# Kernel optimization log

Measured on AMD Instinct MI355X. Metric: run time of the kernel, lower is better.

## Reference

```python
import jax, jax.numpy as jnp
import numpy as np

N_NODES = 100000
N_EDGES = 1600000
D_IN = 64
D_OUT = 64


def setup_inputs() -> dict:
    key = jax.random.key(0)
    k1, k2, k3, k4 = jax.random.split(key, 4)
    x = jax.random.normal(k1, (N_NODES, D_IN), dtype=jnp.float32)
    W = jax.random.normal(k2, (D_OUT, D_IN), dtype=jnp.float32) * 0.1
    b = jax.random.normal(k3, (D_OUT,), dtype=jnp.float32) * 0.1
    edge_index = jax.random.randint(k4, (2, N_EDGES), 0, N_NODES, dtype=jnp.int64 if jax.config.jax_enable_x64 else jnp.int32)
    return {"x": x, "W": W, "b": b, "edge_index": edge_index}


def reference(x, W, b, edge_index):
    N = x.shape[0]
    # add self loops
    loop = jnp.arange(N, dtype=edge_index.dtype)
    src = jnp.concatenate([edge_index[0], loop])  # row: source nodes
    dst = jnp.concatenate([edge_index[1], loop])  # col: target nodes
    E = src.shape[0]

    # linear transform
    h = x @ W.T + b  # [N, D_OUT]

    # degree over source (row) indices, as in the original message()
    ones = jnp.ones((E,), dtype=h.dtype)
    deg = jax.ops.segment_sum(ones, src, num_segments=N)  # [N]
    deg_inv_sqrt = jnp.where(deg > 0, jax.lax.rsqrt(jnp.maximum(deg, 1.0)), 0.0)
    norm = deg_inv_sqrt[src] * deg_inv_sqrt[dst]  # [E]

    # gather-scale messages, then scatter-mean into targets
    msg = norm[:, None] * h[src]  # [E, D_OUT]
    agg_sum = jax.ops.segment_sum(msg, dst, num_segments=N)  # [N, D_OUT]
    cnt = jax.ops.segment_sum(ones, dst, num_segments=N)  # [N]
    out = agg_sum / jnp.maximum(cnt, 1.0)[:, None]
    return out
```

## Files before the change

### kernel.cpp

```cpp
#include <hip/hip_runtime.h>
#include <hip/hip_fp16.h>

#define N_D 64
#define PB_D 6
#define PSZ_D 64
#define CAP_D 1536
#define PB_S 7
#define PSZ_S 128
#define CAP_S 3072

__global__ __launch_bounds__(1024) void scatter_kernel(const int* __restrict__ src,
                                                       const int* __restrict__ dst,
                                                       int* __restrict__ cursorD,
                                                       int* __restrict__ cursorS,
                                                       unsigned* __restrict__ epart,
                                                       unsigned char* __restrict__ spart,
                                                       int E, int PD, int PS) {
    extern __shared__ int sh[];
    int* hD = sh;
    int* hS = sh + PD;
    int* bD = sh + PD + PS;
    int* bS = sh + 2 * PD + PS;
    int t = threadIdx.x;
    for (int i = t; i < PD + PS; i += 1024) sh[i] = 0;
    __syncthreads();
    const int4* src4 = (const int4*)src;
    const int4* dst4 = (const int4*)dst;
    int E4 = E >> 2;
    int per = (E4 + gridDim.x - 1) / gridDim.x;
    int beg = blockIdx.x * per, end = min(E4, beg + per);
    bool tailblk = (blockIdx.x == 0);
    for (int e = beg + t; e < end; e += 1024) {
        int4 d = dst4[e];
        int4 s = src4[e];
        atomicAdd(&hD[d.x >> PB_D], 1);
        atomicAdd(&hD[d.y >> PB_D], 1);
        atomicAdd(&hD[d.z >> PB_D], 1);
        atomicAdd(&hD[d.w >> PB_D], 1);
        atomicAdd(&hS[s.x >> PB_S], 1);
        atomicAdd(&hS[s.y >> PB_S], 1);
        atomicAdd(&hS[s.z >> PB_S], 1);
        atomicAdd(&hS[s.w >> PB_S], 1);
    }
    if (tailblk) {
        for (int e = (E4 << 2) + t; e < E; e += 1024) {
            atomicAdd(&hD[dst[e] >> PB_D], 1);
            atomicAdd(&hS[src[e] >> PB_S], 1);
        }
    }
    __syncthreads();
    for (int p = t; p < PD; p += 1024) {
        int hd = hD[p];
        if (hd) {
            int r = atomicAdd(&cursorD[p], hd);
            if (r > CAP_D - hd) r = max(CAP_D - hd, 0);
            bD[p] = r;
        }
        hD[p] = 0;
    }
    for (int p = t; p < PS; p += 1024) {
        int hs_ = hS[p];
        if (hs_) {
            int r = atomicAdd(&cursorS[p], hs_);
            if (r > CAP_S - hs_) r = max(CAP_S - hs_, 0);
            bS[p] = r;
        }
        hS[p] = 0;
    }
    __syncthreads();
    for (int e = beg + t; e < end; e += 1024) {
        int4 dv = dst4[e];
        int4 sv = src4[e];
        int ds_[4] = {dv.x, dv.y, dv.z, dv.w};
        int ss_[4] = {sv.x, sv.y, sv.z, sv.w};
#pragma unroll
        for (int k = 0; k < 4; k++) {
            int d = ds_[k], s0 = ss_[k];
            int pd = d >> PB_D, ps = s0 >> PB_S;
            int od = atomicAdd(&hD[pd], 1);
            epart[(size_t)pd * CAP_D + bD[pd] + od] =
                ((unsigned)s0 << PB_D) | (unsigned)(d & (PSZ_D - 1));
            int os = atomicAdd(&hS[ps], 1);
            spart[(size_t)ps * CAP_S + bS[ps] + os] = (unsigned char)(s0 & (PSZ_S - 1));
        }
    }
    if (tailblk) {
        for (int e = (E4 << 2) + t; e < E; e += 1024) {
            int d = dst[e], s0 = src[e];
            int pd = d >> PB_D, ps = s0 >> PB_S;
            int od = atomicAdd(&hD[pd], 1);
            epart[(size_t)pd * CAP_D + bD[pd] + od] =
                ((unsigned)s0 << PB_D) | (unsigned)(d & (PSZ_D - 1));
            int os = atomicAdd(&hS[ps], 1);
            spart[(size_t)ps * CAP_S + bS[ps] + os] = (unsigned char)(s0 & (PSZ_S - 1));
        }
    }
}

#define LROWS 128
__global__ __launch_bounds__(256) void linear_kernel(const float* __restrict__ x,
                                                     const float* __restrict__ W,
                                                     const float* __restrict__ b,
                                                     const unsigned char* __restrict__ spart,
                                                     const int* __restrict__ cursorS,
                                                     float* __restrict__ dis,
                                                     __half* __restrict__ hs, int N) {
    __shared__ float xs[LROWS][N_D + 1];
    __shared__ float Wt[N_D][N_D + 4];
    __shared__ float bs[N_D];
    __shared__ int ohist[PSZ_S];
    __shared__ float disS[PSZ_S];

    int tid = threadIdx.x;
    int p = blockIdx.x;
    if (tid < PSZ_S) ohist[tid] = 0;
    for (int i = tid; i < N_D * N_D; i += 256) {
        int o = i >> 6, k = i & 63;
        Wt[k][o] = W[i];
    }
    if (tid < N_D) bs[tid] = b[tid];
    __syncthreads();

    {
        size_t sbase = (size_t)p * CAP_S;
        int len = min(cursorS[p], CAP_S);
        const unsigned* sp4 = (const unsigned*)(spart + sbase);
        int n4 = len >> 2;
        for (int i = tid; i < n4; i += 256) {
            unsigned v = sp4[i];
            atomicAdd(&ohist[v & 127], 1);
            atomicAdd(&ohist[(v >> 8) & 127], 1);
            atomicAdd(&ohist[(v >> 16) & 127], 1);
            atomicAdd(&ohist[(v >> 24) & 127], 1);
        }
        for (int i = (n4 << 2) + tid; i < len; i += 256)
            atomicAdd(&ohist[spart[sbase + i]], 1);
    }

    int row0 = p * LROWS;
    const float4* x4 = (const float4*)(x + (size_t)row0 * N_D);
    const int n4x = LROWS * N_D / 4;
    if (row0 + LROWS <= N) {
        for (int i = tid; i < n4x; i += 256) {
            float4 v = x4[i];
            int r = i >> 4, kq = (i & 15) << 2;
            xs[r][kq] = v.x; xs[r][kq + 1] = v.y; xs[r][kq + 2] = v.z; xs[r][kq + 3] = v.w;
        }
    } else {
        for (int i = tid; i < n4x; i += 256) {
            int r = i >> 4, kq = (i & 15) << 2;
            float4 v = make_float4(0.f, 0.f, 0.f, 0.f);
            if (row0 + r < N) v = x4[i];
            xs[r][kq] = v.x; xs[r][kq + 1] = v.y; xs[r][kq + 2] = v.z; xs[r][kq + 3] = v.w;
        }
    }
    __syncthreads();

    if (tid < PSZ_S) {
        float dv = rsqrtf((float)(ohist[tid] + 1));
        disS[tid] = dv;
        int node = row0 + tid;
        if (node < N) dis[node] = dv;
    }
    __syncthreads();

    int tc = tid >> 5;
    int tr = tid & 31;
    float acc[4][8];
#pragma unroll
    for (int j = 0; j < 4; j++)
#pragma unroll
        for (int i = 0; i < 8; i++) acc[j][i] = 0.f;

#pragma unroll 4
    for (int k = 0; k < N_D; k++) {
        float4 w0 = *(const float4*)&Wt[k][tc * 8];
        float4 w1 = *(const float4*)&Wt[k][tc * 8 + 4];
        float wv[8] = {w0.x, w0.y, w0.z, w0.w, w1.x, w1.y, w1.z, w1.w};
        float xv[4];
#pragma unroll
        for (int j = 0; j < 4; j++) xv[j] = xs[tr + 32 * j][k];
#pragma unroll
        for (int j = 0; j < 4; j++)
#pragma unroll
            for (int i = 0; i < 8; i++) acc[j][i] += xv[j] * wv[i];
    }

#pragma unroll
    for (int j = 0; j < 4; j++) {
        int row = row0 + tr + 32 * j;
        if (row < N) {
            float dr = disS[tr + 32 * j];
            union { __half h[8]; int4 v; } u;
#pragma unroll
            for (int i = 0; i < 8; i++)
                u.h[i] = __float2half_rn((acc[j][i] + bs[tc * 8 + i]) * dr);
            *(int4*)(hs + (size_t)row * N_D + tc * 8) = u.v;
        }
    }
}

__device__ __forceinline__ float hload(const char* hbase, int off, int lane2) {
    return __half2float(*(const __half*)(hbase + (size_t)(unsigned)off + lane2));
}

__global__ __launch_bounds__(256) void gather_part_kernel(const unsigned* __restrict__ epart,
                                                          const int* __restrict__ cursorD,
                                                          const __half* __restrict__ hs,
                                                          const float* __restrict__ dis,
                                                          float* __restrict__ out, int N) {
    __shared__ unsigned raw[CAP_D];
    __shared__ int sorted[CAP_D];
    __shared__ int hist[PSZ_D];
    __shared__ int rs[PSZ_D];
    __shared__ int cur[PSZ_D];
    int p = blockIdx.x, t = threadIdx.x;
    if (t < PSZ_D) hist[t] = 0;
    __syncthreads();
    size_t base = (size_t)p * CAP_D;
    int num = min(cursorD[p], CAP_D);
    {
        const uint4* ep4 = (const uint4*)(epart + base);
        int n4 = num >> 2;
        for (int i4 = t; i4 < n4; i4 += 256) {
            uint4 v = ep4[i4];
            ((uint4*)raw)[i4] = v;
            atomicAdd(&hist[v.x & (PSZ_D - 1)], 1);
            atomicAdd(&hist[v.y & (PSZ_D - 1)], 1);
            atomicAdd(&hist[v.z & (PSZ_D - 1)], 1);
            atomicAdd(&hist[v.w & (PSZ_D - 1)], 1);
        }
        for (int i = (n4 << 2) + t; i < num; i += 256) {
            unsigned e = epart[base + i];
            raw[i] = e;
            atomicAdd(&hist[e & (PSZ_D - 1)], 1);
        }
    }
    __syncthreads();
    int v = 0;
    if (t < PSZ_D) { v = hist[t]; rs[t] = v; }
    __syncthreads();
    for (int off = 1; off < PSZ_D; off <<= 1) {
        int x = 0;
        if (t < PSZ_D && t >= off) x = rs[t - off];
        __syncthreads();
        if (t < PSZ_D) rs[t] += x;
        __syncthreads();
    }
    if (t < PSZ_D) { int ex = rs[t] - v; rs[t] = ex; cur[t] = ex; }
    __syncthreads();
    for (int i = t; i < num; i += 256) {
        unsigned e = raw[i];
        int pos = atomicAdd(&cur[e & (PSZ_D - 1)], 1);
        sorted[pos] = (int)((e & ~(unsigned)(PSZ_D - 1)) << 1);
    }
    __syncthreads();
    int w = t >> 6, lane = t & 63, lane2 = lane << 1;
    const char* hbase = (const char*)hs;
    for (int r = w * 16; r < w * 16 + 16; r++) {
        int node = (p << PB_D) + r;
        if (node >= N) break;
        int jb = rs[r];
        int cnt = hist[r];
        float acc = hload(hbase, node << 7, lane2);
        int j = 0;
        for (; j + 8 <= cnt; j += 8) {
            int o0 = sorted[jb + j + 0], o1 = sorted[jb + j + 1];
            int o2 = sorted[jb + j + 2], o3 = sorted[jb + j + 3];
            int o4 = sorted[jb + j + 4], o5 = sorted[jb + j + 5];
            int o6 = sorted[jb + j + 6], o7 = sorted[jb + j + 7];
            float v0 = hload(hbase, o0, lane2);
            float v1 = hload(hbase, o1, lane2);
            float v2 = hload(hbase, o2, lane2);
            float v3 = hload(hbase, o3, lane2);
            float v4 = hload(hbase, o4, lane2);
            float v5 = hload(hbase, o5, lane2);
            float v6 = hload(hbase, o6, lane2);
            float v7 = hload(hbase, o7, lane2);
            acc += v0; acc += v1; acc += v2; acc += v3;
            acc += v4; acc += v5; acc += v6; acc += v7;
        }
        for (; j < cnt; j++) acc += hload(hbase, sorted[jb + j], lane2);
        out[((size_t)node << 6) + lane] = dis[node] * acc / (float)(cnt + 1);
    }
}

extern "C" void kernel_launch(void* const* d_in, const int* in_sizes, int n_in,
                              void* d_out, int out_size, void* d_ws, size_t ws_size,
                              hipStream_t stream) {
    const float* x = (const float*)d_in[0];
    const float* W = (const float*)d_in[1];
    const float* b = (const float*)d_in[2];
    const int* edge_index = (const int*)d_in[3];

    const int N = in_sizes[0] / N_D;
    const int E = in_sizes[3] / 2;
    const int* src = edge_index;
    const int* dst = edge_index + E;
    float* out = (float*)d_out;

    const int PD = (N + PSZ_D - 1) / PSZ_D;
    const int PS = (N + PSZ_S - 1) / PSZ_S;

    char* ws = (char*)d_ws;
    size_t off = 0;
    __half* hs = (__half*)(ws + off);         off += ((size_t)N * N_D * sizeof(__half) + 15) & ~15ull;
    float* dis = (float*)(ws + off);          off += (size_t)N * sizeof(float);
    unsigned* epart = (unsigned*)(ws + off);  off += (size_t)PD * CAP_D * sizeof(unsigned);
    unsigned char* spart = (unsigned char*)(ws + off); off += (size_t)PS * CAP_S;
    int* cursorD = (int*)(ws + off);          off += (size_t)PD * sizeof(int);
    int* cursorS = (int*)(ws + off);          off += (size_t)PS * sizeof(int);
    (void)ws_size;

    size_t lds_scat = 2u * (PD + PS) * sizeof(int);

    hipMemsetAsync(cursorD, 0, (size_t)(PD + PS) * sizeof(int), stream);

    scatter_kernel<<<256, 1024, lds_scat, stream>>>(src, dst, cursorD, cursorS,
                                                    epart, spart, E, PD, PS);
    linear_kernel<<<PS, 256, 0, stream>>>(x, W, b, spart, cursorS, dis, hs, N);
    gather_part_kernel<<<PD, 256, 0, stream>>>(epart, cursorD, hs, dis, out, N);
}
```

Before: 196.8 us.

## Gather neighbor rows with 16-byte loads split across lane groups

The gather kernel now lets each group of 8 lanes load a full 16-byte chunk of a neighbor's half-precision row, so one wavefront handles 8 neighbors per load instead of one 2-byte element per lane. Partial sums are combined with cross-lane shuffles at the end. Neighbor lists are padded to multiples of 8, using a zero row appended to hs and placing the self-loop entry in the padding. The aim is fewer, wider memory transactions and fewer load instructions, in exchange for padding overhead, shuffle reductions and a larger sorted buffer in LDS.

```diff
diff --git a/kernel.cpp b/kernel.cpp
--- a/kernel.cpp
+++ b/kernel.cpp
@@ -5,6 +5,7 @@
 #define PB_D 6
 #define PSZ_D 64
 #define CAP_D 1536
+#define SCAP  2048
 #define PB_S 7
 #define PSZ_S 128
 #define CAP_S 3072
@@ -113,6 +114,7 @@
 
     int tid = threadIdx.x;
     int p = blockIdx.x;
+    if (p == 0 && tid < 32) ((int*)hs)[(size_t)N * 32 + tid] = 0;
     if (tid < PSZ_S) ohist[tid] = 0;
     for (int i = tid; i < N_D * N_D; i += 256) {
         int o = i >> 6, k = i & 63;
@@ -200,8 +202,13 @@
     }
 }
 
-__device__ __forceinline__ float hload(const char* hbase, int off, int lane2) {
-    return __half2float(*(const __half*)(hbase + (size_t)(unsigned)off + lane2));
+__device__ __forceinline__ void acc8(int4 v, float* a) {
+    union { int i; __half2 h; } u;
+    float2 f;
+    u.i = v.x; f = __half22float2(u.h); a[0] += f.x; a[1] += f.y;
+    u.i = v.y; f = __half22float2(u.h); a[2] += f.x; a[3] += f.y;
+    u.i = v.z; f = __half22float2(u.h); a[4] += f.x; a[5] += f.y;
+    u.i = v.w; f = __half22float2(u.h); a[6] += f.x; a[7] += f.y;
 }
 
 __global__ __launch_bounds__(256) void gather_part_kernel(const unsigned* __restrict__ epart,
@@ -210,7 +217,7 @@
                                                           const float* __restrict__ dis,
                                                           float* __restrict__ out, int N) {
     __shared__ unsigned raw[CAP_D];
-    __shared__ int sorted[CAP_D];
+    __shared__ int sorted[SCAP];
     __shared__ int hist[PSZ_D];
     __shared__ int rs[PSZ_D];
     __shared__ int cur[PSZ_D];
@@ -238,7 +245,7 @@
     }
     __syncthreads();
     int v = 0;
-    if (t < PSZ_D) { v = hist[t]; rs[t] = v; }
+    if (t < PSZ_D) { v = (hist[t] + 8) & ~7; rs[t] = v; }
     __syncthreads();
     for (int off = 1; off < PSZ_D; off <<= 1) {
         int x = 0;
@@ -249,39 +256,60 @@
     }
     if (t < PSZ_D) { int ex = rs[t] - v; rs[t] = ex; cur[t] = ex; }
     __syncthreads();
+    if (t < PSZ_D) {
+        int cnt = hist[t];
+        int pb = rs[t] + cnt;
+        int pad = ((cnt + 8) & ~7) - cnt;
+        sorted[pb] = ((p << PB_D) + t) << 7;
+        const int ZERO_OFF = N << 7;
+        for (int k = 1; k < pad; k++) sorted[pb + k] = ZERO_OFF;
+    }
     for (int i = t; i < num; i += 256) {
         unsigned e = raw[i];
         int pos = atomicAdd(&cur[e & (PSZ_D - 1)], 1);
         sorted[pos] = (int)((e & ~(unsigned)(PSZ_D - 1)) << 1);
     }
     __syncthreads();
-    int w = t >> 6, lane = t & 63, lane2 = lane << 1;
+    int w = t >> 6, lane = t & 63;
+    int g = lane & 7, q = lane >> 3;
+    int qb = q << 4;
     const char* hbase = (const char*)hs;
     for (int r = w * 16; r < w * 16 + 16; r++) {
         int node = (p << PB_D) + r;
         if (node >= N) break;
         int jb = rs[r];
         int cnt = hist[r];
-        float acc = hload(hbase, node << 7, lane2);
+        int cntP = (cnt + 8) & ~7;
+        float a[8];
+#pragma unroll
+        for (int i = 0; i < 8; i++) a[i] = 0.f;
         int j = 0;
-        for (; j + 8 <= cnt; j += 8) {
-            int o0 = sorted[jb + j + 0], o1 = sorted[jb + j + 1];
-            int o2 = sorted[jb + j + 2], o3 = sorted[jb + j + 3];
-            int o4 = sorted[jb + j + 4], o5 = sorted[jb + j + 5];
-            int o6 = sorted[jb + j + 6], o7 = sorted[jb + j + 7];
-            float v0 = hload(hbase, o0, lane2);
-            float v1 = hload(hbase, o1, lane2);
-            float v2 = hload(hbase, o2, lane2);
-            float v3 = hload(hbase, o3, lane2);
-            float v4 = hload(hbase, o4, lane2);
-            float v5 = hload(hbase, o5, lane2);
-            float v6 = hload(hbase, o6, lane2);
-            float v7 = hload(hbase, o7, lane2);
-            acc += v0; acc += v1; acc += v2; acc += v3;
-            acc += v4; acc += v5; acc += v6; acc += v7;
-        }
-        for (; j < cnt; j++) acc += hload(hbase, sorted[jb + j], lane2);
-        out[((size_t)node << 6) + lane] = dis[node] * acc / (float)(cnt + 1);
+        for (; j + 16 <= cntP; j += 16) {
+            int o0 = sorted[jb + j + g];
+            int o1 = sorted[jb + j + 8 + g];
+            int4 v0 = *(const int4*)(hbase + (size_t)(unsigned)(o0 + qb));
+            int4 v1 = *(const int4*)(hbase + (size_t)(unsigned)(o1 + qb));
+            acc8(v0, a);
+            acc8(v1, a);
+        }
+        for (; j < cntP; j += 8) {
+            int o = sorted[jb + j + g];
+            int4 v0 = *(const int4*)(hbase + (size_t)(unsigned)(o + qb));
+            acc8(v0, a);
+        }
+#pragma unroll
+        for (int m = 1; m <= 4; m <<= 1) {
+#pragma unroll
+            for (int i = 0; i < 8; i++) a[i] += __shfl_xor(a[i], m, 64);
+        }
+        float scale = dis[node] / (float)(cnt + 1);
+        if (g == 0) {
+            float4 w0 = make_float4(a[0] * scale, a[1] * scale, a[2] * scale, a[3] * scale);
+            float4 w1 = make_float4(a[4] * scale, a[5] * scale, a[6] * scale, a[7] * scale);
+            float4* op = (float4*)(out + ((size_t)node << 6) + (q << 3));
+            op[0] = w0;
+            op[1] = w1;
+        }
     }
 }
 
@@ -304,7 +332,7 @@
 
     char* ws = (char*)d_ws;
     size_t off = 0;
-    __half* hs = (__half*)(ws + off);         off += ((size_t)N * N_D * sizeof(__half) + 15) & ~15ull;
+    __half* hs = (__half*)(ws + off);         off += ((size_t)(N + 1) * N_D * sizeof(__half) + 15) & ~15ull;
     float* dis = (float*)(ws + off);          off += (size_t)N * sizeof(float);
     unsigned* epart = (unsigned*)(ws + off);  off += (size_t)PD * CAP_D * sizeof(unsigned);
     unsigned char* spart = (unsigned char*)(ws + off); off += (size_t)PS * CAP_S;
```

New measurement: 187.1 us. 4.9% less time.
